# Kernel tuning notes

Measured on AMD Instinct MI355X. Metric: run time of the kernel, lower is better.

## Reference

```python
import jax, jax.numpy as jnp
import numpy as np

B, N, C_IN, C_OUT, K = 16, 16384, 128, 128, 9


def setup_inputs() -> dict:
    key = jax.random.key(0)
    ks = jax.random.split(key, 7)
    x = jax.random.normal(ks[0], (B, N, C_IN), dtype=jnp.float32)
    indices = jax.random.randint(ks[1], (N, K), 0, N, dtype=jnp.int32)
    # P initialized near identity (as in the torch module) plus small noise
    P = jnp.eye(K, dtype=jnp.float32)[None].repeat(N, axis=0) \
        + 0.02 * jax.random.normal(ks[2], (N, K, K), dtype=jnp.float32)
    W_conv = jax.random.normal(ks[3], (C_OUT, K * C_IN), dtype=jnp.float32) * (1.0 / np.sqrt(K * C_IN))
    b_conv = jax.random.normal(ks[4], (C_OUT,), dtype=jnp.float32) * 0.01
    W_skip = jax.random.normal(ks[5], (C_OUT, C_IN), dtype=jnp.float32) * (1.0 / np.sqrt(C_IN))
    b_skip = jax.random.normal(ks[6], (C_OUT,), dtype=jnp.float32) * 0.01
    return {"x": x, "indices": indices, "P": P, "W_conv": W_conv,
            "b_conv": b_conv, "W_skip": W_skip, "b_skip": b_skip}


def reference(x, indices, P, W_conv, b_conv, W_skip, b_skip):
    b, n, c = x.shape
    k = P.shape[-1]
    # pad node axis with k zero rows (matches x_padded in torch module)
    x_pad = jnp.concatenate([x, jnp.zeros((b, k, c), dtype=x.dtype)], axis=1)
    # gather k neighbours per node: (b, n, k, c)
    nbr = jnp.take(x_pad, indices, axis=1)
    # per-node kxk permutation/mixing matmul: P (n,k,k) @ nbr (b,n,k,c)
    perm = jnp.einsum('nkj,bnjc->bnkc', P, nbr)
    flat = jax.nn.elu(perm.reshape(b, n, k * c))
    z = jax.nn.elu(jnp.einsum('bnf,of->bno', flat, W_conv) + b_conv)
    # skip connection
    z = jnp.einsum('bnc,oc->bno', x, W_skip) + b_skip + z
    return z
```

## Files before the change

### kernel.cpp

```cpp
#include <hip/hip_runtime.h>
#include <hip/hip_fp16.h>
#include <math.h>

#define B_ 16
#define N_ 16384
#define C_ 128
#define K_ 9
#define FCONV 1152
#define G_ 2
#define FPAD 1160
#define LDS_BYTES (G_ * B_ * FPAD * 2)

typedef _Float16 half8 __attribute__((ext_vector_type(8)));
typedef _Float16 half2v __attribute__((ext_vector_type(2)));
typedef float floatx4 __attribute__((ext_vector_type(4)));

__device__ __forceinline__ float elu_f(float v) {
    return v > 0.f ? v : (__expf(v) - 1.f);
}

__global__ __launch_bounds__(1024) void prep(
    const float* __restrict__ x, const float* __restrict__ Wc, const float* __restrict__ Ws,
    _Float16* __restrict__ x16, _Float16* __restrict__ WcF, _Float16* __restrict__ WsF)
{
    const int t = blockIdx.x * 1024 + threadIdx.x;
    const int NX8 = B_ * N_ * C_ / 8;
    if (t < NX8) {
        const floatx4* px = (const floatx4*)x + (size_t)t * 2;
        const floatx4 a = __builtin_nontemporal_load(px);
        const floatx4 b = __builtin_nontemporal_load(px + 1);
        half8 h = {(_Float16)a.x, (_Float16)a.y, (_Float16)a.z, (_Float16)a.w,
                   (_Float16)b.x, (_Float16)b.y, (_Float16)b.z, (_Float16)b.w};
        *(half8*)(x16 + (size_t)t * 8) = h;
    } else {
        const int i = t - NX8;
        if (i < 8 * 36 * 64 * 8) {
            const int j = i & 7, lane = (i >> 3) & 63;
            const int rest = i >> 9;
            const int kc = rest % 36, ot = rest / 36;
            WcF[i] = (_Float16)Wc[(size_t)(ot * 16 + (lane & 15)) * FCONV + kc * 32 + (lane >> 4) * 8 + j];
        } else {
            const int i2 = i - 8 * 36 * 64 * 8;
            if (i2 < 8 * 4 * 64 * 8) {
                const int j = i2 & 7, lane = (i2 >> 3) & 63;
                const int rest = i2 >> 9;
                const int kc = rest & 3, ot = rest >> 2;
                WsF[i2] = (_Float16)Ws[(size_t)(ot * 16 + (lane & 15)) * C_ + kc * 32 + (lane >> 4) * 8 + j];
            }
        }
    }
}

__global__ __launch_bounds__(512, 4) void paiconv_mfma512(
    const _Float16* __restrict__ x16,
    const int*      __restrict__ idx,
    const float*    __restrict__ P,
    const _Float16* __restrict__ WcF,
    const float*    __restrict__ bc,
    const _Float16* __restrict__ WsF,
    const float*    __restrict__ bs,
    float*          __restrict__ out)
{
    extern __shared__ _Float16 flat_s[];

    const int tid = threadIdx.x;
    const int n0  = blockIdx.x * G_;

    {
        const int cp = tid & 63;
        const int mw = tid >> 6;

        int id0[K_], id1[K_];
        #pragma unroll
        for (int j = 0; j < K_; ++j) id0[j] = idx[(size_t)n0 * K_ + j];
        #pragma unroll
        for (int j = 0; j < K_; ++j) id1[j] = idx[(size_t)(n0 + 1) * K_ + j];

        half2v vp[2][2][K_];
        #pragma unroll
        for (int mi = 0; mi < 2; ++mi) {
            const _Float16* xb = x16 + (size_t)(mw + mi * 8) * (N_ * C_) + 2 * cp;
            #pragma unroll
            for (int j = 0; j < K_; ++j)
                vp[0][mi][j] = *(const half2v*)(xb + (size_t)id0[j] * C_);
            #pragma unroll
            for (int j = 0; j < K_; ++j)
                vp[1][mi][j] = *(const half2v*)(xb + (size_t)id1[j] * C_);
        }

        #pragma unroll
        for (int g = 0; g < G_; ++g) {
            const float* Pn = P + (size_t)(n0 + g) * 81;
            #pragma unroll
            for (int mi = 0; mi < 2; ++mi) {
                const int m = mw + mi * 8;
                float vx[K_], vy[K_];
                #pragma unroll
                for (int j = 0; j < K_; ++j) {
                    vx[j] = (float)vp[g][mi][j][0];
                    vy[j] = (float)vp[g][mi][j][1];
                }
                _Float16* fg = &flat_s[g * (B_ * FPAD) + m * FPAD + 2 * cp];
                #pragma unroll
                for (int k = 0; k < K_; ++k) {
                    float s0 = 0.f, s1 = 0.f;
                    #pragma unroll
                    for (int j = 0; j < K_; ++j) {
                        const float p = Pn[k * K_ + j];
                        s0 = fmaf(p, vx[j], s0);
                        s1 = fmaf(p, vy[j], s1);
                    }
                    half2v r = {(_Float16)elu_f(s0), (_Float16)elu_f(s1)};
                    *(half2v*)&fg[k * C_] = r;
                }
            }
        }
    }

    const int w    = tid >> 6;
    const int lane = tid & 63;
    const int col  = lane & 15;
    const int quad = lane >> 4;
    const int o0   = w * 16;

    const half8* WcF8 = (const half8*)WcF + (size_t)w * 36 * 64 + lane;
    const half8* WsF8 = (const half8*)WsF + (size_t)w * 4 * 64 + lane;

    half8 sb[4], sa0[4], sa1[4], bq[8];
    #pragma unroll
    for (int k4 = 0; k4 < 4; ++k4) {
        sb[k4]  = WsF8[k4 * 64];
        sa0[k4] = *(const half8*)(x16 + ((size_t)col * N_ + n0) * C_ + k4 * 32 + quad * 8);
        sa1[k4] = *(const half8*)(x16 + ((size_t)col * N_ + n0 + 1) * C_ + k4 * 32 + quad * 8);
    }
    #pragma unroll
    for (int p = 0; p < 8; ++p) bq[p] = WcF8[p * 64];

    __syncthreads();

    floatx4 accS0 = (floatx4){0.f, 0.f, 0.f, 0.f};
    floatx4 accS1 = (floatx4){0.f, 0.f, 0.f, 0.f};
    #pragma unroll
    for (int k4 = 0; k4 < 4; ++k4) {
        accS0 = __builtin_amdgcn_mfma_f32_16x16x32_f16(sa0[k4], sb[k4], accS0, 0, 0, 0);
        accS1 = __builtin_amdgcn_mfma_f32_16x16x32_f16(sa1[k4], sb[k4], accS1, 0, 0, 0);
    }

    const _Float16* fg0 = &flat_s[col * FPAD];
    const _Float16* fg1 = &flat_s[B_ * FPAD + col * FPAD];
    floatx4 accC0 = (floatx4){0.f, 0.f, 0.f, 0.f};
    floatx4 accC1 = (floatx4){0.f, 0.f, 0.f, 0.f};

    half8 a0q[4], a1q[4];
    #pragma unroll
    for (int p = 0; p < 4; ++p) {
        a0q[p] = *(const half8*)&fg0[p * 32 + quad * 8];
        a1q[p] = *(const half8*)&fg1[p * 32 + quad * 8];
    }
    #pragma unroll
    for (int k = 0; k < 36; ++k) {
        const half8 b  = bq[k & 7];
        const half8 a0 = a0q[k & 3];
        const half8 a1 = a1q[k & 3];
        if (k + 8 < 36) bq[k & 7] = WcF8[(k + 8) * 64];
        if (k + 4 < 36) {
            a0q[k & 3] = *(const half8*)&fg0[(k + 4) * 32 + quad * 8];
            a1q[k & 3] = *(const half8*)&fg1[(k + 4) * 32 + quad * 8];
        }
        accC0 = __builtin_amdgcn_mfma_f32_16x16x32_f16(a0, b, accC0, 0, 0, 0);
        accC1 = __builtin_amdgcn_mfma_f32_16x16x32_f16(a1, b, accC1, 0, 0, 0);
    }

    const float bcv = bc[o0 + col];
    const float bsv = bs[o0 + col];
    #pragma unroll
    for (int r = 0; r < 4; ++r) {
        const int m = quad * 4 + r;
        const float z0 = elu_f(accC0[r] + bcv) + accS0[r] + bsv;
        const float z1 = elu_f(accC1[r] + bcv) + accS1[r] + bsv;
        __builtin_nontemporal_store(z0, &out[((size_t)m * N_ + n0) * C_ + o0 + col]);
        __builtin_nontemporal_store(z1, &out[((size_t)m * N_ + n0 + 1) * C_ + o0 + col]);
    }
}

__global__ void build_wfrag(const float* __restrict__ Wc, const float* __restrict__ Ws,
                            _Float16* __restrict__ WcF, _Float16* __restrict__ WsF) {
    const int i = blockIdx.x * 256 + threadIdx.x;
    if (i < 8 * 36 * 64 * 8) {
        const int j = i & 7, lane = (i >> 3) & 63;
        const int rest = i >> 9;
        const int kc = rest % 36, ot = rest / 36;
        WcF[i] = (_Float16)Wc[(size_t)(ot * 16 + (lane & 15)) * FCONV + kc * 32 + (lane >> 4) * 8 + j];
    }
    if (i < 8 * 4 * 64 * 8) {
        const int j = i & 7, lane = (i >> 3) & 63;
        const int rest = i >> 9;
        const int kc = rest & 3, ot = rest >> 2;
        WsF[i] = (_Float16)Ws[(size_t)(ot * 16 + (lane & 15)) * C_ + kc * 32 + (lane >> 4) * 8 + j];
    }
}

template <bool WF16>
__global__ __launch_bounds__(1024, 8) void paiconv_legacy(
    const float* __restrict__ x, const int* __restrict__ idx, const float* __restrict__ P,
    const void* __restrict__ WcP, const float* __restrict__ bc,
    const void* __restrict__ WsP, const float* __restrict__ bs, float* __restrict__ out)
{
    extern __shared__ _Float16 flat_s[];
    const int tid = threadIdx.x;
    const int n0  = blockIdx.x * G_;
    {
        const int cp = tid & 63;
        const int m  = tid >> 6;
        #pragma unroll
        for (int g = 0; g < G_; ++g) {
            const int n = n0 + g;
            int id[K_];
            #pragma unroll
            for (int j = 0; j < K_; ++j) id[j] = idx[(size_t)n * K_ + j];
            float vx[K_], vy[K_];
            #pragma unroll
            for (int j = 0; j < K_; ++j) {
                const bool ok = (unsigned)id[j] < (unsigned)N_;
                const float* q = x + ((size_t)m * N_ + id[j]) * C_ + 2 * cp;
                float2 h = ok ? *(const float2*)q : (float2){0.f, 0.f};
                vx[j] = h.x; vy[j] = h.y;
            }
            const float* Pn = P + (size_t)n * 81;
            _Float16* fg = &flat_s[g * (B_ * FPAD) + m * FPAD + 2 * cp];
            #pragma unroll
            for (int k = 0; k < K_; ++k) {
                float s0 = 0.f, s1 = 0.f;
                #pragma unroll
                for (int j = 0; j < K_; ++j) {
                    const float p = Pn[k * K_ + j];
                    s0 = fmaf(p, vx[j], s0);
                    s1 = fmaf(p, vy[j], s1);
                }
                half2v r = {(_Float16)elu_f(s0), (_Float16)elu_f(s1)};
                *(half2v*)&fg[k * C_] = r;
            }
        }
    }
    __syncthreads();

    const int w = tid >> 6, lane = tid & 63;
    const int col = lane & 15, quad = lane >> 4;
    const int g = w & 1, ot = w >> 1, o0 = ot * 16;
    const int n = n0 + g;

    floatx4 accC = (floatx4){0.f, 0.f, 0.f, 0.f};
    floatx4 accS = (floatx4){0.f, 0.f, 0.f, 0.f};

    for (int k0 = 0; k0 < C_; k0 += 32) {
        const float* p = x + ((size_t)col * N_ + n) * C_ + k0 + quad * 8;
        const float4 x0 = *(const float4*)p;
        const float4 x1 = *(const float4*)(p + 4);
        half8 a = (half8){(_Float16)x0.x, (_Float16)x0.y, (_Float16)x0.z, (_Float16)x0.w,
                          (_Float16)x1.x, (_Float16)x1.y, (_Float16)x1.z, (_Float16)x1.w};
        half8 b;
        if (WF16) {
            b = ((const half8*)WsP)[(ot * 4 + (k0 >> 5)) * 64 + lane];
        } else {
            const float* q = (const float*)WsP + (size_t)(o0 + col) * C_ + k0 + quad * 8;
            const float4 w0 = *(const float4*)q;
            const float4 w1 = *(const float4*)(q + 4);
            b = (half8){(_Float16)w0.x, (_Float16)w0.y, (_Float16)w0.z, (_Float16)w0.w,
                        (_Float16)w1.x, (_Float16)w1.y, (_Float16)w1.z, (_Float16)w1.w};
        }
        accS = __builtin_amdgcn_mfma_f32_16x16x32_f16(a, b, accS, 0, 0, 0);
    }
    const _Float16* fg = &flat_s[g * (B_ * FPAD) + col * FPAD];
    for (int k0 = 0; k0 < FCONV; k0 += 32) {
        half8 a = *(const half8*)&fg[k0 + quad * 8];
        half8 b;
        if (WF16) {
            b = ((const half8*)WcP)[(ot * 36 + (k0 >> 5)) * 64 + lane];
        } else {
            const float* q = (const float*)WcP + (size_t)(o0 + col) * FCONV + k0 + quad * 8;
            const float4 w0 = *(const float4*)q;
            const float4 w1 = *(const float4*)(q + 4);
            b = (half8){(_Float16)w0.x, (_Float16)w0.y, (_Float16)w0.z, (_Float16)w0.w,
                        (_Float16)w1.x, (_Float16)w1.y, (_Float16)w1.z, (_Float16)w1.w};
        }
        accC = __builtin_amdgcn_mfma_f32_16x16x32_f16(a, b, accC, 0, 0, 0);
    }
    const float bcv = bc[o0 + col];
    const float bsv = bs[o0 + col];
    #pragma unroll
    for (int r = 0; r < 4; ++r) {
        const int m = quad * 4 + r;
        const float z = elu_f(accC[r] + bcv);
        __builtin_nontemporal_store(z + accS[r] + bsv, &out[((size_t)m * N_ + n) * C_ + o0 + col]);
    }
}

extern "C" void kernel_launch(void* const* d_in, const int* in_sizes, int n_in,
                              void* d_out, int out_size, void* d_ws, size_t ws_size,
                              hipStream_t stream) {
    const float* x   = (const float*)d_in[0];
    const int*   idx = (const int*)  d_in[1];
    const float* P   = (const float*)d_in[2];
    const float* Wc  = (const float*)d_in[3];
    const float* bc  = (const float*)d_in[4];
    const float* Ws  = (const float*)d_in[5];
    const float* bs  = (const float*)d_in[6];
    float* out = (float*)d_out;

    const size_t x16_halfs = (size_t)B_ * N_ * C_;
    const size_t wc_halfs  = (size_t)8 * 36 * 64 * 8;
    const size_t wsk_halfs = (size_t)8 * 4 * 64 * 8;
    const size_t need_full = (x16_halfs + wc_halfs + wsk_halfs) * sizeof(_Float16);
    const size_t need_w    = (wc_halfs + wsk_halfs) * sizeof(_Float16);

    if (ws_size >= need_full) {
        _Float16* x16 = (_Float16*)d_ws;
        _Float16* WcF = x16 + x16_halfs;
        _Float16* WsF = WcF + wc_halfs;
        prep<<<dim3(4256), dim3(1024), 0, stream>>>(x, Wc, Ws, x16, WcF, WsF);
        hipFuncSetAttribute((const void*)paiconv_mfma512,
                            hipFuncAttributeMaxDynamicSharedMemorySize, LDS_BYTES);
        paiconv_mfma512<<<dim3(N_ / G_), dim3(512), LDS_BYTES, stream>>>(
            x16, idx, P, WcF, bc, WsF, bs, out);
    } else if (ws_size >= need_w) {
        _Float16* WcF = (_Float16*)d_ws;
        _Float16* WsF = WcF + wc_halfs;
        build_wfrag<<<dim3(576), dim3(256), 0, stream>>>(Wc, Ws, WcF, WsF);
        hipFuncSetAttribute((const void*)paiconv_legacy<true>,
                            hipFuncAttributeMaxDynamicSharedMemorySize, LDS_BYTES);
        paiconv_legacy<true><<<dim3(N_ / G_), dim3(1024), LDS_BYTES, stream>>>(
            x, idx, P, WcF, bc, WsF, bs, out);
    } else {
        hipFuncSetAttribute((const void*)paiconv_legacy<false>,
                            hipFuncAttributeMaxDynamicSharedMemorySize, LDS_BYTES);
        paiconv_legacy<false><<<dim3(N_ / G_), dim3(1024), LDS_BYTES, stream>>>(
            x, idx, P, Wc, bc, Ws, bs, out);
    }
}
```

Before: 501.9 us.

## Process one node per 256-thread block with two output tiles per wave

Replaces the two-node, 512-thread block with a one-node, 256-thread block. Each wave now computes two 16-wide output tiles against one shared A fragment, so it reuses A from LDS instead of reusing the weight fragment across two nodes. LDS per block is halved and twice as many blocks are launched. In exchange, each conv weight fragment is now loaded from global/L2 once per node rather than once per two nodes, which roughly doubles weight traffic. The permutation step also uses packed float2 FMAs.

```diff
diff --git a/kernel.cpp b/kernel.cpp
--- a/kernel.cpp
+++ b/kernel.cpp
@@ -7,13 +7,15 @@
 #define C_ 128
 #define K_ 9
 #define FCONV 1152
+#define FPAD 1160
+#define LDS1_BYTES (B_ * FPAD * 2)
 #define G_ 2
-#define FPAD 1160
-#define LDS_BYTES (G_ * B_ * FPAD * 2)
+#define LDS2_BYTES (G_ * B_ * FPAD * 2)
 
 typedef _Float16 half8 __attribute__((ext_vector_type(8)));
 typedef _Float16 half2v __attribute__((ext_vector_type(2)));
 typedef float floatx4 __attribute__((ext_vector_type(4)));
+typedef float floatx2 __attribute__((ext_vector_type(2)));
 
 __device__ __forceinline__ float elu_f(float v) {
     return v > 0.f ? v : (__expf(v) - 1.f);
@@ -51,7 +53,7 @@
     }
 }
 
-__global__ __launch_bounds__(512, 4) void paiconv_mfma512(
+__global__ __launch_bounds__(256, 4) void paiconv_g1(
     const _Float16* __restrict__ x16,
     const int*      __restrict__ idx,
     const float*    __restrict__ P,
@@ -64,55 +66,41 @@
     extern __shared__ _Float16 flat_s[];
 
     const int tid = threadIdx.x;
-    const int n0  = blockIdx.x * G_;
+    const int n   = blockIdx.x;
 
     {
         const int cp = tid & 63;
         const int mw = tid >> 6;
 
-        int id0[K_], id1[K_];
+        int id[K_];
         #pragma unroll
-        for (int j = 0; j < K_; ++j) id0[j] = idx[(size_t)n0 * K_ + j];
+        for (int j = 0; j < K_; ++j) id[j] = idx[(size_t)n * K_ + j];
+
+        half2v vp[4][K_];
         #pragma unroll
-        for (int j = 0; j < K_; ++j) id1[j] = idx[(size_t)(n0 + 1) * K_ + j];
-
-        half2v vp[2][2][K_];
+        for (int mi = 0; mi < 4; ++mi) {
+            const _Float16* xb = x16 + (size_t)(mw * 4 + mi) * (N_ * C_) + 2 * cp;
+            #pragma unroll
+            for (int j = 0; j < K_; ++j)
+                vp[mi][j] = *(const half2v*)(xb + (size_t)id[j] * C_);
+        }
+
+        const float* Pn = P + (size_t)n * 81;
         #pragma unroll
-        for (int mi = 0; mi < 2; ++mi) {
-            const _Float16* xb = x16 + (size_t)(mw + mi * 8) * (N_ * C_) + 2 * cp;
+        for (int mi = 0; mi < 4; ++mi) {
+            floatx2 v[K_];
             #pragma unroll
             for (int j = 0; j < K_; ++j)
-                vp[0][mi][j] = *(const half2v*)(xb + (size_t)id0[j] * C_);
-            #pragma unroll
-            for (int j = 0; j < K_; ++j)
-                vp[1][mi][j] = *(const half2v*)(xb + (size_t)id1[j] * C_);
-        }
-
-        #pragma unroll
-        for (int g = 0; g < G_; ++g) {
-            const float* Pn = P + (size_t)(n0 + g) * 81;
-            #pragma unroll
-            for (int mi = 0; mi < 2; ++mi) {
-                const int m = mw + mi * 8;
-                float vx[K_], vy[K_];
+                v[j] = (floatx2){(float)vp[mi][j][0], (float)vp[mi][j][1]};
+            _Float16* fg = &flat_s[(mw * 4 + mi) * FPAD + 2 * cp];
+            #pragma unroll
+            for (int k = 0; k < K_; ++k) {
+                floatx2 s = (floatx2){0.f, 0.f};
                 #pragma unroll
-                for (int j = 0; j < K_; ++j) {
-                    vx[j] = (float)vp[g][mi][j][0];
-                    vy[j] = (float)vp[g][mi][j][1];
-                }
-                _Float16* fg = &flat_s[g * (B_ * FPAD) + m * FPAD + 2 * cp];
-                #pragma unroll
-                for (int k = 0; k < K_; ++k) {
-                    float s0 = 0.f, s1 = 0.f;
-                    #pragma unroll
-                    for (int j = 0; j < K_; ++j) {
-                        const float p = Pn[k * K_ + j];
-                        s0 = fmaf(p, vx[j], s0);
-                        s1 = fmaf(p, vy[j], s1);
-                    }
-                    half2v r = {(_Float16)elu_f(s0), (_Float16)elu_f(s1)};
-                    *(half2v*)&fg[k * C_] = r;
-                }
+                for (int j = 0; j < K_; ++j)
+                    s += Pn[k * K_ + j] * v[j];
+                half2v r = {(_Float16)elu_f(s.x), (_Float16)elu_f(s.y)};
+                *(half2v*)&fg[k * C_] = r;
             }
         }
     }
@@ -121,20 +109,25 @@
     const int lane = tid & 63;
     const int col  = lane & 15;
     const int quad = lane >> 4;
-    const int o0   = w * 16;
-
-    const half8* WcF8 = (const half8*)WcF + (size_t)w * 36 * 64 + lane;
-    const half8* WsF8 = (const half8*)WsF + (size_t)w * 4 * 64 + lane;
-
-    half8 sb[4], sa0[4], sa1[4], bq[8];
+    const int ot0  = 2 * w, ot1 = 2 * w + 1;
+
+    const half8* Wc0 = (const half8*)WcF + (size_t)ot0 * 36 * 64 + lane;
+    const half8* Wc1 = (const half8*)WcF + (size_t)ot1 * 36 * 64 + lane;
+    const half8* Ws0 = (const half8*)WsF + (size_t)ot0 * 4 * 64 + lane;
+    const half8* Ws1 = (const half8*)WsF + (size_t)ot1 * 4 * 64 + lane;
+
+    half8 sb0[4], sb1[4], sa[4], b0q[4], b1q[4];
     #pragma unroll
     for (int k4 = 0; k4 < 4; ++k4) {
-        sb[k4]  = WsF8[k4 * 64];
-        sa0[k4] = *(const half8*)(x16 + ((size_t)col * N_ + n0) * C_ + k4 * 32 + quad * 8);
-        sa1[k4] = *(const half8*)(x16 + ((size_t)col * N_ + n0 + 1) * C_ + k4 * 32 + quad * 8);
-    }
-    #pragma unroll
-    for (int p = 0; p < 8; ++p) bq[p] = WcF8[p * 64];
+        sb0[k4] = Ws0[k4 * 64];
+        sb1[k4] = Ws1[k4 * 64];
+        sa[k4]  = *(const half8*)(x16 + ((size_t)col * N_ + n) * C_ + k4 * 32 + quad * 8);
+    }
+    #pragma unroll
+    for (int p = 0; p < 4; ++p) {
+        b0q[p] = Wc0[p * 64];
+        b1q[p] = Wc1[p * 64];
+    }
 
     __syncthreads();
 
@@ -142,44 +135,42 @@
     floatx4 accS1 = (floatx4){0.f, 0.f, 0.f, 0.f};
     #pragma unroll
     for (int k4 = 0; k4 < 4; ++k4) {
-        accS0 = __builtin_amdgcn_mfma_f32_16x16x32_f16(sa0[k4], sb[k4], accS0, 0, 0, 0);
-        accS1 = __builtin_amdgcn_mfma_f32_16x16x32_f16(sa1[k4], sb[k4], accS1, 0, 0, 0);
-    }
-
-    const _Float16* fg0 = &flat_s[col * FPAD];
-    const _Float16* fg1 = &flat_s[B_ * FPAD + col * FPAD];
+        accS0 = __builtin_amdgcn_mfma_f32_16x16x32_f16(sa[k4], sb0[k4], accS0, 0, 0, 0);
+        accS1 = __builtin_amdgcn_mfma_f32_16x16x32_f16(sa[k4], sb1[k4], accS1, 0, 0, 0);
+    }
+
+    const _Float16* fg = &flat_s[col * FPAD];
     floatx4 accC0 = (floatx4){0.f, 0.f, 0.f, 0.f};
     floatx4 accC1 = (floatx4){0.f, 0.f, 0.f, 0.f};
 
-    half8 a0q[4], a1q[4];
-    #pragma unroll
-    for (int p = 0; p < 4; ++p) {
-        a0q[p] = *(const half8*)&fg0[p * 32 + quad * 8];
-        a1q[p] = *(const half8*)&fg1[p * 32 + quad * 8];
-    }
+    half8 aq[4];
+    #pragma unroll
+    for (int p = 0; p < 4; ++p)
+        aq[p] = *(const half8*)&fg[p * 32 + quad * 8];
+
     #pragma unroll
     for (int k = 0; k < 36; ++k) {
-        const half8 b  = bq[k & 7];
-        const half8 a0 = a0q[k & 3];
-        const half8 a1 = a1q[k & 3];
-        if (k + 8 < 36) bq[k & 7] = WcF8[(k + 8) * 64];
+        const half8 a  = aq[k & 3];
+        const half8 b0 = b0q[k & 3];
+        const half8 b1 = b1q[k & 3];
         if (k + 4 < 36) {
-            a0q[k & 3] = *(const half8*)&fg0[(k + 4) * 32 + quad * 8];
-            a1q[k & 3] = *(const half8*)&fg1[(k + 4) * 32 + quad * 8];
-        }
-        accC0 = __builtin_amdgcn_mfma_f32_16x16x32_f16(a0, b, accC0, 0, 0, 0);
-        accC1 = __builtin_amdgcn_mfma_f32_16x16x32_f16(a1, b, accC1, 0, 0, 0);
-    }
-
-    const float bcv = bc[o0 + col];
-    const float bsv = bs[o0 + col];
+            aq[k & 3]  = *(const half8*)&fg[(k + 4) * 32 + quad * 8];
+            b0q[k & 3] = Wc0[(k + 4) * 64];
+            b1q[k & 3] = Wc1[(k + 4) * 64];
+        }
+        accC0 = __builtin_amdgcn_mfma_f32_16x16x32_f16(a, b0, accC0, 0, 0, 0);
+        accC1 = __builtin_amdgcn_mfma_f32_16x16x32_f16(a, b1, accC1, 0, 0, 0);
+    }
+
+    const float bc0 = bc[ot0 * 16 + col], bc1 = bc[ot1 * 16 + col];
+    const float bs0 = bs[ot0 * 16 + col], bs1 = bs[ot1 * 16 + col];
     #pragma unroll
     for (int r = 0; r < 4; ++r) {
         const int m = quad * 4 + r;
-        const float z0 = elu_f(accC0[r] + bcv) + accS0[r] + bsv;
-        const float z1 = elu_f(accC1[r] + bcv) + accS1[r] + bsv;
-        __builtin_nontemporal_store(z0, &out[((size_t)m * N_ + n0) * C_ + o0 + col]);
-        __builtin_nontemporal_store(z1, &out[((size_t)m * N_ + n0 + 1) * C_ + o0 + col]);
+        const float z0 = elu_f(accC0[r] + bc0) + accS0[r] + bs0;
+        const float z1 = elu_f(accC1[r] + bc1) + accS1[r] + bs1;
+        __builtin_nontemporal_store(z0, &out[((size_t)m * N_ + n) * C_ + ot0 * 16 + col]);
+        __builtin_nontemporal_store(z1, &out[((size_t)m * N_ + n) * C_ + ot1 * 16 + col]);
     }
 }
 
@@ -318,22 +309,22 @@
         _Float16* WcF = x16 + x16_halfs;
         _Float16* WsF = WcF + wc_halfs;
         prep<<<dim3(4256), dim3(1024), 0, stream>>>(x, Wc, Ws, x16, WcF, WsF);
-        hipFuncSetAttribute((const void*)paiconv_mfma512,
-                            hipFuncAttributeMaxDynamicSharedMemorySize, LDS_BYTES);
-        paiconv_mfma512<<<dim3(N_ / G_), dim3(512), LDS_BYTES, stream>>>(
+        hipFuncSetAttribute((const void*)paiconv_g1,
+                            hipFuncAttributeMaxDynamicSharedMemorySize, LDS1_BYTES);
+        paiconv_g1<<<dim3(N_), dim3(256), LDS1_BYTES, stream>>>(
             x16, idx, P, WcF, bc, WsF, bs, out);
     } else if (ws_size >= need_w) {
         _Float16* WcF = (_Float16*)d_ws;
         _Float16* WsF = WcF + wc_halfs;
         build_wfrag<<<dim3(576), dim3(256), 0, stream>>>(Wc, Ws, WcF, WsF);
         hipFuncSetAttribute((const void*)paiconv_legacy<true>,
-                            hipFuncAttributeMaxDynamicSharedMemorySize, LDS_BYTES);
-        paiconv_legacy<true><<<dim3(N_ / G_), dim3(1024), LDS_BYTES, stream>>>(
+                            hipFuncAttributeMaxDynamicSharedMemorySize, LDS2_BYTES);
+        paiconv_legacy<true><<<dim3(N_ / G_), dim3(1024), LDS2_BYTES, stream>>>(
             x, idx, P, WcF, bc, WsF, bs, out);
     } else {
         hipFuncSetAttribute((const void*)paiconv_legacy<false>,
-                            hipFuncAttributeMaxDynamicSharedMemorySize, LDS_BYTES);
-        paiconv_legacy<false><<<dim3(N_ / G_), dim3(1024), LDS_BYTES, stream>>>(
+                            hipFuncAttributeMaxDynamicSharedMemorySize, LDS2_BYTES);
+        paiconv_legacy<false><<<dim3(N_ / G_), dim3(1024), LDS2_BYTES, stream>>>(
             x, idx, P, Wc, bc, Ws, bs, out);
     }
 }
```

Measured after the change: 667.4 us. 33.0% more time.
